# Performance work log

Hardware: AMD Instinct MI355X
Metric: run time of the kernel (lower is better)

The kernel has to match this reference:

```python
import jax, jax.numpy as jnp
import numpy as np

NEG_BIG = -9.0e15

def setup_inputs() -> dict:
    key = jax.random.key(0)
    k1, k2, k3, k4 = jax.random.split(key, 4)
    N, F_in, F_out = 2048, 512, 64
    x = jax.random.normal(k1, (N, F_in), dtype=jnp.float32)
    adj = jax.random.randint(k2, (N, N), 0, 2, dtype=jnp.int32)
    # xavier_uniform with gain=1.414
    def xavier(k, shape, gain=1.414):
        fan_in, fan_out = shape[0], shape[1]
        bound = gain * np.sqrt(6.0 / (fan_in + fan_out))
        return jax.random.uniform(k, shape, jnp.float32, -bound, bound)
    W = xavier(k3, (F_in, F_out))
    a = xavier(k4, (F_out, 1))
    return {"x": x, "adj": adj, "W": W, "a": a}

def reference(x, adj, W, a):
    h = x @ W                                  # [N, F_out]
    # pairwise |h_i - h_j| projected by a: e[i,j] = relu(sum_f |h_i,f - h_j,f| * a_f)
    diff = jnp.abs(h[:, None, :] - h[None, :, :])   # [N, N, F_out]
    e = jax.nn.relu(jnp.einsum('ijf,fo->ij', diff, a))  # [N, N]
    scores = jnp.where(adj > 0, e, NEG_BIG)
    attention = jax.nn.softmax(scores, axis=1)
    out = attention @ h                        # [N, F_out]
    return jax.nn.relu(out)                    # concat=True path
```

## Files before the change

### kernel.cpp

```cpp
#include <hip/hip_runtime.h>

#define Nn 2048
#define FIN 512
#define FO 64
#define SHIFT 20.0f
#define NSEG 4
#define SEGJ (Nn / NSEG)
#define CH 64
#define LST 66
#define PSTRIDE 68

__global__ __launch_bounds__(256) void gat_xw(const float* __restrict__ x,
                                              const float* __restrict__ W,
                                              float* __restrict__ h) {
    __shared__ float part[2][2][FO];
    const int wave = threadIdx.x >> 6;
    const int lane = threadIdx.x & 63;
    const int rs = wave >> 1;
    const int kh = wave & 1;
    int row = blockIdx.x * 2 + rs;
    row = __builtin_amdgcn_readfirstlane(row);
    const float* xr = x + (size_t)row * FIN + kh * (FIN / 2);
    const float* Wp = W + (size_t)kh * (FIN / 2) * FO;
    float acc = 0.f;
#pragma unroll 2
    for (int k = 0; k < FIN / 2; k += 8) {
        float4 xa = *(const float4*)(xr + k);
        float4 xb = *(const float4*)(xr + k + 4);
        acc = fmaf(xa.x, Wp[(k + 0) * FO + lane], acc);
        acc = fmaf(xa.y, Wp[(k + 1) * FO + lane], acc);
        acc = fmaf(xa.z, Wp[(k + 2) * FO + lane], acc);
        acc = fmaf(xa.w, Wp[(k + 3) * FO + lane], acc);
        acc = fmaf(xb.x, Wp[(k + 4) * FO + lane], acc);
        acc = fmaf(xb.y, Wp[(k + 5) * FO + lane], acc);
        acc = fmaf(xb.z, Wp[(k + 6) * FO + lane], acc);
        acc = fmaf(xb.w, Wp[(k + 7) * FO + lane], acc);
    }
    part[rs][kh][lane] = acc;
    __syncthreads();
    if (threadIdx.x < 128) {
        const int r2 = threadIdx.x >> 6;
        const int l2 = threadIdx.x & 63;
        h[((size_t)blockIdx.x * 2 + r2) * FO + l2] = part[r2][0][l2] + part[r2][1][l2];
    }
}

__global__ __launch_bounds__(256) void gat_attn(const float* __restrict__ h,
                                                const int* __restrict__ adj,
                                                const float* __restrict__ a,
                                                float* __restrict__ pws) {
    __shared__ float hj[CH * LST];
    __shared__ float hia[4 * FO * 2];
    const int tid = threadIdx.x;
    const int wave = tid >> 6;
    const int lane = tid & 63;
    const int seg = blockIdx.x & (NSEG - 1);
    const int row = (blockIdx.x >> 2) * 4 + wave;

    hia[wave * (FO * 2) + lane * 2]     = h[(size_t)row * FO + lane];
    hia[wave * (FO * 2) + lane * 2 + 1] = a[lane];

    float l = 0.f;
    float2 op2[32];
#pragma unroll
    for (int q = 0; q < 32; q++) op2[q] = make_float2(0.f, 0.f);

    const int* adjrow = adj + (size_t)row * Nn + seg * SEGJ;
    const float* hseg = h + (size_t)seg * SEGJ * FO;

    for (int j0 = 0; j0 < SEGJ; j0 += CH) {
        __syncthreads();
#pragma unroll
        for (int u = 0; u < 4; u++) {
            const int g4 = u * 256 + tid;
            const float4 v = *(const float4*)(hseg + (size_t)j0 * FO + (size_t)g4 * 4);
            float* dst = &hj[(g4 >> 4) * LST + (g4 & 15) * 4];
            ((float2*)dst)[0] = make_float2(v.x, v.y);
            *(float2*)(dst + 2) = make_float2(v.z, v.w);
        }
        __syncthreads();

        const int av = adjrow[j0 + lane];

        float2 hjv[32];
#pragma unroll
        for (int q = 0; q < 32; q++)
            hjv[q] = *(const float2*)&hj[lane * LST + q * 2];

        float e = 0.f;
#pragma unroll
        for (int q = 0; q < 32; q++) {
            const float4 c = *(const float4*)&hia[wave * (FO * 2) + q * 4];
            e = fmaf(fabsf(hjv[q].x - c.x), c.y, e);
            e = fmaf(fabsf(hjv[q].y - c.z), c.w, e);
        }

        const float pe = __expf(fmaxf(e, 0.f) - SHIFT);
        const float p = (av > 0) ? pe : 0.f;
        l += p;

#pragma unroll
        for (int q = 0; q < 32; q++) {
            op2[q].x = fmaf(p, hjv[q].x, op2[q].x);
            op2[q].y = fmaf(p, hjv[q].y, op2[q].y);
        }
    }

#pragma unroll
    for (int s = 32; s >= 1; s >>= 1) l += __shfl_xor(l, s, 64);
#pragma unroll
    for (int q = 0; q < 32; q++) {
        op2[q].x += __shfl_xor(op2[q].x, 16, 64);
        op2[q].x += __shfl_xor(op2[q].x, 32, 64);
        op2[q].y += __shfl_xor(op2[q].y, 16, 64);
        op2[q].y += __shfl_xor(op2[q].y, 32, 64);
    }
    __syncthreads();
    float* red = &hj[wave * (16 * 65)];
    if (lane < 16) {
#pragma unroll
        for (int q = 0; q < 32; q++) {
            red[lane * 65 + 2 * q]     = op2[q].x;
            red[lane * 65 + 2 * q + 1] = op2[q].y;
        }
    }
    float tot = 0.f;
#pragma unroll
    for (int g = 0; g < 16; g++)
        tot += red[g * 65 + lane];
    float* prow = pws + ((size_t)seg * Nn + row) * PSTRIDE;
    prow[lane] = tot;
    if (lane == 0) prow[FO] = l;
}

__global__ __launch_bounds__(256) void gat_merge(const float* __restrict__ pws,
                                                 float* __restrict__ out) {
    const int t = blockIdx.x * 256 + threadIdx.x;
    const int row = t >> 6;
    const int f = t & 63;
    float o = 0.f, l = 0.f;
#pragma unroll
    for (int s = 0; s < NSEG; s++) {
        const float* pr = pws + ((size_t)s * Nn + row) * PSTRIDE;
        o += pr[f];
        l += pr[FO];
    }
    out[t] = fmaxf(o / l, 0.f);
}

extern "C" void kernel_launch(void* const* d_in, const int* in_sizes, int n_in,
                              void* d_out, int out_size, void* d_ws, size_t ws_size,
                              hipStream_t stream) {
    const float* x   = (const float*)d_in[0];
    const int*   adj = (const int*)d_in[1];
    const float* W   = (const float*)d_in[2];
    const float* a   = (const float*)d_in[3];
    float* out = (float*)d_out;
    float* h   = (float*)d_ws;
    float* pws = (float*)d_ws + (size_t)Nn * FO;

    gat_xw<<<dim3(1024), dim3(256), 0, stream>>>(x, W, h);
    gat_attn<<<dim3(512 * NSEG), dim3(256), 0, stream>>>(h, adj, a, pws);
    gat_merge<<<dim3(512), dim3(256), 0, stream>>>(pws, out);
}
```

Baseline: 143.1 us.

## Register-tile attention as 64x128 i-j blocks with atomic accumulation

Replaces the one-row-per-wave attention kernel with a 2D tiled kernel. Each block owns 64 query rows and a 128-column key range, each thread computes a 4x4 patch of scores, and the probabilities are staged transposed in shared memory for a 4x4 register-tiled P·H product. This raises reuse of the h_i and h_j values loaded from shared memory, where the old code re-read every h_j once per row. Partial sums from the 16 column tiles go into global buffers through atomicAdd, after a new zeroing kernel clears them. The cost is an extra launch, atomic contention, float-order nondeterminism, and fewer blocks (512), which may leave the machine underfilled.

```diff
diff --git a/kernel.cpp b/kernel.cpp
--- a/kernel.cpp
+++ b/kernel.cpp
@@ -4,11 +4,14 @@
 #define FIN 512
 #define FO 64
 #define SHIFT 20.0f
-#define NSEG 4
-#define SEGJ (Nn / NSEG)
-#define CH 64
-#define LST 66
-#define PSTRIDE 68
+#define NJT 16
+#define JR (Nn / NJT)
+#define LS 66
+#define PTS 68
+
+__global__ __launch_bounds__(256) void gat_zero(float* __restrict__ z) {
+    z[blockIdx.x * 256 + threadIdx.x] = 0.f;
+}
 
 __global__ __launch_bounds__(256) void gat_xw(const float* __restrict__ x,
                                               const float* __restrict__ W,
@@ -45,107 +48,153 @@
     }
 }
 
-__global__ __launch_bounds__(256) void gat_attn(const float* __restrict__ h,
-                                                const int* __restrict__ adj,
-                                                const float* __restrict__ a,
-                                                float* __restrict__ pws) {
-    __shared__ float hj[CH * LST];
-    __shared__ float hia[4 * FO * 2];
+__global__ __launch_bounds__(256) void gat_attn3(const float* __restrict__ h,
+                                                 const int* __restrict__ adj,
+                                                 const float* __restrict__ a,
+                                                 float* __restrict__ osum,
+                                                 float* __restrict__ lsum) {
+    __shared__ float hi_s[64 * LS];
+    __shared__ float hj_s[64 * LS];
+    __shared__ float pT_s[64 * PTS];
+    __shared__ float a_s[FO];
+
     const int tid = threadIdx.x;
-    const int wave = tid >> 6;
+    const int w = tid >> 6;
     const int lane = tid & 63;
-    const int seg = blockIdx.x & (NSEG - 1);
-    const int row = (blockIdx.x >> 2) * 4 + wave;
-
-    hia[wave * (FO * 2) + lane * 2]     = h[(size_t)row * FO + lane];
-    hia[wave * (FO * 2) + lane * 2 + 1] = a[lane];
-
-    float l = 0.f;
-    float2 op2[32];
-#pragma unroll
-    for (int q = 0; q < 32; q++) op2[q] = make_float2(0.f, 0.f);
-
-    const int* adjrow = adj + (size_t)row * Nn + seg * SEGJ;
-    const float* hseg = h + (size_t)seg * SEGJ * FO;
-
-    for (int j0 = 0; j0 < SEGJ; j0 += CH) {
+    const int li = lane & 3;
+    const int lj = lane >> 2;
+    const int it = blockIdx.x >> 4;
+    const int jt = blockIdx.x & (NJT - 1);
+    const int ib = it * 64;
+    const int jb = jt * JR;
+    const int iw = w * 16;
+
+    for (int g4 = tid; g4 < 1024; g4 += 256) {
+        float4 v = *(const float4*)(h + (size_t)ib * FO + (size_t)g4 * 4);
+        float* d = &hi_s[(g4 >> 4) * LS + (g4 & 15) * 4];
+        *(float2*)d = make_float2(v.x, v.y);
+        *(float2*)(d + 2) = make_float2(v.z, v.w);
+    }
+    if (tid < FO) a_s[tid] = a[tid];
+
+    float pv[4][4];
+    float ls[4];
+#pragma unroll
+    for (int u = 0; u < 4; u++) {
+        ls[u] = 0.f;
+#pragma unroll
+        for (int v2 = 0; v2 < 4; v2++) pv[u][v2] = 0.f;
+    }
+
+    for (int jc = 0; jc < JR; jc += 64) {
         __syncthreads();
-#pragma unroll
-        for (int u = 0; u < 4; u++) {
-            const int g4 = u * 256 + tid;
-            const float4 v = *(const float4*)(hseg + (size_t)j0 * FO + (size_t)g4 * 4);
-            float* dst = &hj[(g4 >> 4) * LST + (g4 & 15) * 4];
-            ((float2*)dst)[0] = make_float2(v.x, v.y);
-            *(float2*)(dst + 2) = make_float2(v.z, v.w);
+        const float* hsrc = h + (size_t)(jb + jc) * FO;
+        for (int g4 = tid; g4 < 1024; g4 += 256) {
+            float4 v = *(const float4*)(hsrc + (size_t)g4 * 4);
+            float* d = &hj_s[(g4 >> 4) * LS + (g4 & 15) * 4];
+            *(float2*)d = make_float2(v.x, v.y);
+            *(float2*)(d + 2) = make_float2(v.z, v.w);
         }
         __syncthreads();
 
-        const int av = adjrow[j0 + lane];
-
-        float2 hjv[32];
-#pragma unroll
-        for (int q = 0; q < 32; q++)
-            hjv[q] = *(const float2*)&hj[lane * LST + q * 2];
-
-        float e = 0.f;
-#pragma unroll
-        for (int q = 0; q < 32; q++) {
-            const float4 c = *(const float4*)&hia[wave * (FO * 2) + q * 4];
-            e = fmaf(fabsf(hjv[q].x - c.x), c.y, e);
-            e = fmaf(fabsf(hjv[q].y - c.z), c.w, e);
-        }
-
-        const float pe = __expf(fmaxf(e, 0.f) - SHIFT);
-        const float p = (av > 0) ? pe : 0.f;
-        l += p;
-
-#pragma unroll
-        for (int q = 0; q < 32; q++) {
-            op2[q].x = fmaf(p, hjv[q].x, op2[q].x);
-            op2[q].y = fmaf(p, hjv[q].y, op2[q].y);
-        }
-    }
-
-#pragma unroll
-    for (int s = 32; s >= 1; s >>= 1) l += __shfl_xor(l, s, 64);
-#pragma unroll
-    for (int q = 0; q < 32; q++) {
-        op2[q].x += __shfl_xor(op2[q].x, 16, 64);
-        op2[q].x += __shfl_xor(op2[q].x, 32, 64);
-        op2[q].y += __shfl_xor(op2[q].y, 16, 64);
-        op2[q].y += __shfl_xor(op2[q].y, 32, 64);
-    }
-    __syncthreads();
-    float* red = &hj[wave * (16 * 65)];
-    if (lane < 16) {
-#pragma unroll
-        for (int q = 0; q < 32; q++) {
-            red[lane * 65 + 2 * q]     = op2[q].x;
-            red[lane * 65 + 2 * q + 1] = op2[q].y;
-        }
-    }
-    float tot = 0.f;
-#pragma unroll
-    for (int g = 0; g < 16; g++)
-        tot += red[g * 65 + lane];
-    float* prow = pws + ((size_t)seg * Nn + row) * PSTRIDE;
-    prow[lane] = tot;
-    if (lane == 0) prow[FO] = l;
-}
-
-__global__ __launch_bounds__(256) void gat_merge(const float* __restrict__ pws,
-                                                 float* __restrict__ out) {
+        int4 am[4];
+#pragma unroll
+        for (int di = 0; di < 4; di++)
+            am[di] = *(const int4*)(adj + (size_t)(ib + iw + 4 * li + di) * Nn + (jb + jc + 4 * lj));
+
+        float e[4][4];
+#pragma unroll
+        for (int di = 0; di < 4; di++)
+#pragma unroll
+            for (int dj = 0; dj < 4; dj++) e[di][dj] = 0.f;
+
+#pragma unroll 4
+        for (int f = 0; f < FO; f += 2) {
+            const float2 av = *(const float2*)&a_s[f];
+            float2 hi[4], hj[4];
+#pragma unroll
+            for (int d = 0; d < 4; d++) {
+                hi[d] = *(const float2*)&hi_s[(iw + 4 * li + d) * LS + f];
+                hj[d] = *(const float2*)&hj_s[(4 * lj + d) * LS + f];
+            }
+#pragma unroll
+            for (int di = 0; di < 4; di++)
+#pragma unroll
+                for (int dj = 0; dj < 4; dj++) {
+                    e[di][dj] = fmaf(fabsf(hi[di].x - hj[dj].x), av.x, e[di][dj]);
+                    e[di][dj] = fmaf(fabsf(hi[di].y - hj[dj].y), av.y, e[di][dj]);
+                }
+        }
+
+#pragma unroll
+        for (int di = 0; di < 4; di++) {
+            const int* ap = (const int*)&am[di];
+#pragma unroll
+            for (int dj = 0; dj < 4; dj++) {
+                const float p = (ap[dj] > 0) ? __expf(fmaxf(e[di][dj], 0.f) - SHIFT) : 0.f;
+                e[di][dj] = p;
+                ls[di] += p;
+            }
+        }
+
+#pragma unroll
+        for (int dj = 0; dj < 4; dj++) {
+            *(float4*)&pT_s[(4 * lj + dj) * PTS + iw + 4 * li] =
+                make_float4(e[0][dj], e[1][dj], e[2][dj], e[3][dj]);
+        }
+        __syncthreads();
+
+#pragma unroll 4
+        for (int j = 0; j < 64; j++) {
+            const float4 pj = *(const float4*)&pT_s[j * PTS + iw + 4 * li];
+            const float2 h0 = *(const float2*)&hj_s[j * LS + 4 * lj];
+            const float2 h1 = *(const float2*)&hj_s[j * LS + 4 * lj + 2];
+            pv[0][0] = fmaf(pj.x, h0.x, pv[0][0]);
+            pv[0][1] = fmaf(pj.x, h0.y, pv[0][1]);
+            pv[0][2] = fmaf(pj.x, h1.x, pv[0][2]);
+            pv[0][3] = fmaf(pj.x, h1.y, pv[0][3]);
+            pv[1][0] = fmaf(pj.y, h0.x, pv[1][0]);
+            pv[1][1] = fmaf(pj.y, h0.y, pv[1][1]);
+            pv[1][2] = fmaf(pj.y, h1.x, pv[1][2]);
+            pv[1][3] = fmaf(pj.y, h1.y, pv[1][3]);
+            pv[2][0] = fmaf(pj.z, h0.x, pv[2][0]);
+            pv[2][1] = fmaf(pj.z, h0.y, pv[2][1]);
+            pv[2][2] = fmaf(pj.z, h1.x, pv[2][2]);
+            pv[2][3] = fmaf(pj.z, h1.y, pv[2][3]);
+            pv[3][0] = fmaf(pj.w, h0.x, pv[3][0]);
+            pv[3][1] = fmaf(pj.w, h0.y, pv[3][1]);
+            pv[3][2] = fmaf(pj.w, h1.x, pv[3][2]);
+            pv[3][3] = fmaf(pj.w, h1.y, pv[3][3]);
+        }
+    }
+
+#pragma unroll
+    for (int di = 0; di < 4; di++) {
+        float v = ls[di];
+        v += __shfl_xor(v, 4, 64);
+        v += __shfl_xor(v, 8, 64);
+        v += __shfl_xor(v, 16, 64);
+        v += __shfl_xor(v, 32, 64);
+        ls[di] = v;
+    }
+    if (lj == 0) {
+#pragma unroll
+        for (int di = 0; di < 4; di++)
+            atomicAdd(&lsum[ib + iw + 4 * li + di], ls[di]);
+    }
+#pragma unroll
+    for (int di = 0; di < 4; di++) {
+#pragma unroll
+        for (int v2 = 0; v2 < 4; v2++)
+            atomicAdd(&osum[(size_t)(ib + iw + 4 * li + di) * FO + 4 * lj + v2], pv[di][v2]);
+    }
+}
+
+__global__ __launch_bounds__(256) void gat_fin(const float* __restrict__ osum,
+                                               const float* __restrict__ lsum,
+                                               float* __restrict__ out) {
     const int t = blockIdx.x * 256 + threadIdx.x;
-    const int row = t >> 6;
-    const int f = t & 63;
-    float o = 0.f, l = 0.f;
-#pragma unroll
-    for (int s = 0; s < NSEG; s++) {
-        const float* pr = pws + ((size_t)s * Nn + row) * PSTRIDE;
-        o += pr[f];
-        l += pr[FO];
-    }
-    out[t] = fmaxf(o / l, 0.f);
+    out[t] = fmaxf(osum[t] / lsum[t >> 6], 0.f);
 }
 
 extern "C" void kernel_launch(void* const* d_in, const int* in_sizes, int n_in,
@@ -156,10 +205,13 @@
     const float* W   = (const float*)d_in[2];
     const float* a   = (const float*)d_in[3];
     float* out = (float*)d_out;
-    float* h   = (float*)d_ws;
-    float* pws = (float*)d_ws + (size_t)Nn * FO;
-
+
+    float* h    = (float*)d_ws;
+    float* osum = h + (size_t)Nn * FO;
+    float* lsum = osum + (size_t)Nn * FO;
+
+    gat_zero<<<dim3(520), dim3(256), 0, stream>>>(osum);
     gat_xw<<<dim3(1024), dim3(256), 0, stream>>>(x, W, h);
-    gat_attn<<<dim3(512 * NSEG), dim3(256), 0, stream>>>(h, adj, a, pws);
-    gat_merge<<<dim3(512), dim3(256), 0, stream>>>(pws, out);
-}
+    gat_attn3<<<dim3(32 * NJT), dim3(256), 0, stream>>>(h, adj, a, osum, lsum);
+    gat_fin<<<dim3(512), dim3(256), 0, stream>>>(osum, lsum, out);
+}
```

Result: faster. 136.2 us (-4.8%).

## Tile attention over i×j blocks and compute P·H with split-bf16 MFMA

Applied to the files above, without the earlier changes.

Rewrites the attention kernel so each block handles a 16-row by 1024-column tile. Each thread computes scores for 8 rows by 2 columns, so every h_j loaded from swizzled LDS is reused across rows. The P·H product runs on bf16 MFMA using a hi/lo split (three MFMAs) to approximate fp32 accuracy. A new transpose kernel precomputes H^T in hi/lo bf16, and the merge now combines two column halves instead of four. The grid drops to 256 blocks, which risks underfilling the GPU, and h_i is read from global memory inside the inner loop.

```diff
diff --git a/kernel.cpp b/kernel.cpp
--- a/kernel.cpp
+++ b/kernel.cpp
@@ -4,11 +4,18 @@
 #define FIN 512
 #define FO 64
 #define SHIFT 20.0f
-#define NSEG 4
-#define SEGJ (Nn / NSEG)
-#define CH 64
-#define LST 66
-#define PSTRIDE 68
+#define NJT 2
+#define JSEG 1024
+#define CHK 256
+
+typedef __attribute__((ext_vector_type(8))) short bf16x8;
+typedef __attribute__((ext_vector_type(4))) float f32x4;
+
+__device__ __forceinline__ unsigned rne_bf16(float x) {
+    unsigned u = __float_as_uint(x);
+    return (u + 0x7FFFu + ((u >> 16) & 1u)) >> 16;
+}
+__device__ __forceinline__ float bf16_f32(unsigned s) { return __uint_as_float(s << 16); }
 
 __global__ __launch_bounds__(256) void gat_xw(const float* __restrict__ x,
                                               const float* __restrict__ W,
@@ -45,106 +52,145 @@
     }
 }
 
-__global__ __launch_bounds__(256) void gat_attn(const float* __restrict__ h,
-                                                const int* __restrict__ adj,
-                                                const float* __restrict__ a,
-                                                float* __restrict__ pws) {
-    __shared__ float hj[CH * LST];
-    __shared__ float hia[4 * FO * 2];
+__global__ __launch_bounds__(256) void gat_tr(const float* __restrict__ h,
+                                              unsigned short* __restrict__ hbT_hi,
+                                              unsigned short* __restrict__ hbT_lo) {
+    __shared__ float t_s[64 * 68];
     const int tid = threadIdx.x;
-    const int wave = tid >> 6;
+    const int j0 = blockIdx.x * 64;
+    for (int g4 = tid; g4 < 1024; g4 += 256) {
+        float4 v = *(const float4*)(h + (size_t)j0 * FO + (size_t)g4 * 4);
+        *(float4*)&t_s[(g4 >> 4) * 68 + (g4 & 15) * 4] = v;
+    }
+    __syncthreads();
+    const int f = tid >> 2, q = tid & 3;
+    unsigned* dh = (unsigned*)&hbT_hi[(size_t)f * Nn + j0 + q * 16];
+    unsigned* dl = (unsigned*)&hbT_lo[(size_t)f * Nn + j0 + q * 16];
+#pragma unroll
+    for (int u = 0; u < 8; u++) {
+        float x0 = t_s[(q * 16 + 2 * u) * 68 + f];
+        float x1 = t_s[(q * 16 + 2 * u + 1) * 68 + f];
+        unsigned h0 = rne_bf16(x0), h1 = rne_bf16(x1);
+        dh[u] = h0 | (h1 << 16);
+        float r0 = x0 - bf16_f32(h0), r1 = x1 - bf16_f32(h1);
+        dl[u] = rne_bf16(r0) | (rne_bf16(r1) << 16);
+    }
+}
+
+__global__ __launch_bounds__(256) void gat_attn7(const float* __restrict__ h,
+                                                 const int* __restrict__ adj,
+                                                 const float* __restrict__ a,
+                                                 const unsigned short* __restrict__ hbT_hi,
+                                                 const unsigned short* __restrict__ hbT_lo,
+                                                 float* __restrict__ opart,
+                                                 float* __restrict__ lpart) {
+    __shared__ float hj_s[CHK * 64];
+    __shared__ unsigned short Ph_s[16 * 264];
+    __shared__ unsigned short Pl_s[16 * 264];
+
+    const int tid = threadIdx.x;
+    const int it = blockIdx.x >> 1;
+    const int jt = blockIdx.x & 1;
+    const int ib = it * 16;
+    const int jb = jt * JSEG;
+    const int ig = __builtin_amdgcn_readfirstlane(tid >> 7);
+    const int jg = tid & 127;
     const int lane = tid & 63;
-    const int seg = blockIdx.x & (NSEG - 1);
-    const int row = (blockIdx.x >> 2) * 4 + wave;
-
-    hia[wave * (FO * 2) + lane * 2]     = h[(size_t)row * FO + lane];
-    hia[wave * (FO * 2) + lane * 2 + 1] = a[lane];
-
-    float l = 0.f;
-    float2 op2[32];
-#pragma unroll
-    for (int q = 0; q < 32; q++) op2[q] = make_float2(0.f, 0.f);
-
-    const int* adjrow = adj + (size_t)row * Nn + seg * SEGJ;
-    const float* hseg = h + (size_t)seg * SEGJ * FO;
-
-    for (int j0 = 0; j0 < SEGJ; j0 += CH) {
+    const int w = tid >> 6;
+    const int m = lane & 15;
+    const int g = lane >> 4;
+
+    float ls[8] = {0.f, 0.f, 0.f, 0.f, 0.f, 0.f, 0.f, 0.f};
+    f32x4 acc = {0.f, 0.f, 0.f, 0.f};
+
+    for (int jc = 0; jc < JSEG; jc += CHK) {
         __syncthreads();
-#pragma unroll
-        for (int u = 0; u < 4; u++) {
-            const int g4 = u * 256 + tid;
-            const float4 v = *(const float4*)(hseg + (size_t)j0 * FO + (size_t)g4 * 4);
-            float* dst = &hj[(g4 >> 4) * LST + (g4 & 15) * 4];
-            ((float2*)dst)[0] = make_float2(v.x, v.y);
-            *(float2*)(dst + 2) = make_float2(v.z, v.w);
+        const float* hsrc = h + (size_t)(jb + jc) * FO;
+        for (int g4 = tid; g4 < 4096; g4 += 256) {
+            const int j = g4 >> 4, c = g4 & 15;
+            *(float4*)&hj_s[j * 64 + ((c ^ (j & 7)) << 2)] =
+                *(const float4*)(hsrc + (size_t)g4 * 4);
         }
         __syncthreads();
 
-        const int av = adjrow[j0 + lane];
-
-        float2 hjv[32];
-#pragma unroll
-        for (int q = 0; q < 32; q++)
-            hjv[q] = *(const float2*)&hj[lane * LST + q * 2];
-
-        float e = 0.f;
-#pragma unroll
-        for (int q = 0; q < 32; q++) {
-            const float4 c = *(const float4*)&hia[wave * (FO * 2) + q * 4];
-            e = fmaf(fabsf(hjv[q].x - c.x), c.y, e);
-            e = fmaf(fabsf(hjv[q].y - c.z), c.w, e);
-        }
-
-        const float pe = __expf(fmaxf(e, 0.f) - SHIFT);
-        const float p = (av > 0) ? pe : 0.f;
-        l += p;
-
-#pragma unroll
-        for (int q = 0; q < 32; q++) {
-            op2[q].x = fmaf(p, hjv[q].x, op2[q].x);
-            op2[q].y = fmaf(p, hjv[q].y, op2[q].y);
-        }
-    }
-
-#pragma unroll
-    for (int s = 32; s >= 1; s >>= 1) l += __shfl_xor(l, s, 64);
-#pragma unroll
-    for (int q = 0; q < 32; q++) {
-        op2[q].x += __shfl_xor(op2[q].x, 16, 64);
-        op2[q].x += __shfl_xor(op2[q].x, 32, 64);
-        op2[q].y += __shfl_xor(op2[q].y, 16, 64);
-        op2[q].y += __shfl_xor(op2[q].y, 32, 64);
-    }
-    __syncthreads();
-    float* red = &hj[wave * (16 * 65)];
-    if (lane < 16) {
-#pragma unroll
-        for (int q = 0; q < 32; q++) {
-            red[lane * 65 + 2 * q]     = op2[q].x;
-            red[lane * 65 + 2 * q + 1] = op2[q].y;
-        }
-    }
-    float tot = 0.f;
-#pragma unroll
-    for (int g = 0; g < 16; g++)
-        tot += red[g * 65 + lane];
-    float* prow = pws + ((size_t)seg * Nn + row) * PSTRIDE;
-    prow[lane] = tot;
-    if (lane == 0) prow[FO] = l;
-}
-
-__global__ __launch_bounds__(256) void gat_merge(const float* __restrict__ pws,
+        const int j0 = jg * 2, j1 = j0 + 1;
+        int2 am[8];
+        const int* adjp = adj + (size_t)(ib + ig * 8) * Nn + (jb + jc + j0);
+#pragma unroll
+        for (int ii = 0; ii < 8; ii++) am[ii] = *(const int2*)(adjp + (size_t)ii * Nn);
+
+        float e[8][2];
+#pragma unroll
+        for (int ii = 0; ii < 8; ii++) e[ii][0] = e[ii][1] = 0.f;
+
+#pragma unroll 2
+        for (int fq = 0; fq < 16; fq++) {
+            const int f = fq * 4;
+            const float4 av = *(const float4*)(a + f);
+            const float4 hj0 = *(const float4*)&hj_s[j0 * 64 + ((fq ^ (j0 & 7)) << 2)];
+            const float4 hj1 = *(const float4*)&hj_s[j1 * 64 + ((fq ^ (j1 & 7)) << 2)];
+#pragma unroll
+            for (int ii = 0; ii < 8; ii++) {
+                const float4 hi = *(const float4*)(h + (size_t)(ib + ig * 8 + ii) * FO + f);
+                e[ii][0] = fmaf(fabsf(hi.x - hj0.x), av.x, e[ii][0]);
+                e[ii][0] = fmaf(fabsf(hi.y - hj0.y), av.y, e[ii][0]);
+                e[ii][0] = fmaf(fabsf(hi.z - hj0.z), av.z, e[ii][0]);
+                e[ii][0] = fmaf(fabsf(hi.w - hj0.w), av.w, e[ii][0]);
+                e[ii][1] = fmaf(fabsf(hi.x - hj1.x), av.x, e[ii][1]);
+                e[ii][1] = fmaf(fabsf(hi.y - hj1.y), av.y, e[ii][1]);
+                e[ii][1] = fmaf(fabsf(hi.z - hj1.z), av.z, e[ii][1]);
+                e[ii][1] = fmaf(fabsf(hi.w - hj1.w), av.w, e[ii][1]);
+            }
+        }
+
+#pragma unroll
+        for (int ii = 0; ii < 8; ii++) {
+            const float p0 = (am[ii].x > 0) ? __expf(fmaxf(e[ii][0], 0.f) - SHIFT) : 0.f;
+            const float p1 = (am[ii].y > 0) ? __expf(fmaxf(e[ii][1], 0.f) - SHIFT) : 0.f;
+            ls[ii] += p0 + p1;
+            const unsigned h0 = rne_bf16(p0), h1 = rne_bf16(p1);
+            const float r0 = p0 - bf16_f32(h0), r1 = p1 - bf16_f32(h1);
+            ((unsigned*)Ph_s)[(ig * 8 + ii) * 132 + jg] = h0 | (h1 << 16);
+            ((unsigned*)Pl_s)[(ig * 8 + ii) * 132 + jg] =
+                rne_bf16(r0) | (rne_bf16(r1) << 16);
+        }
+        __syncthreads();
+
+        const size_t bbase = (size_t)(w * 16 + m) * Nn + (jb + jc);
+#pragma unroll
+        for (int ks = 0; ks < 8; ks++) {
+            const bf16x8 af = *(const bf16x8*)&Ph_s[m * 264 + ks * 32 + g * 8];
+            const bf16x8 al = *(const bf16x8*)&Pl_s[m * 264 + ks * 32 + g * 8];
+            const bf16x8 bh = *(const bf16x8*)&hbT_hi[bbase + ks * 32 + g * 8];
+            const bf16x8 bl = *(const bf16x8*)&hbT_lo[bbase + ks * 32 + g * 8];
+            acc = __builtin_amdgcn_mfma_f32_16x16x32_bf16(af, bh, acc, 0, 0, 0);
+            acc = __builtin_amdgcn_mfma_f32_16x16x32_bf16(af, bl, acc, 0, 0, 0);
+            acc = __builtin_amdgcn_mfma_f32_16x16x32_bf16(al, bh, acc, 0, 0, 0);
+        }
+    }
+
+    __syncthreads();
+    float* red = hj_s;
+#pragma unroll
+    for (int ii = 0; ii < 8; ii++) red[(ig * 8 + ii) * 132 + jg] = ls[ii];
+    __syncthreads();
+    if (tid < 16) {
+        float l = 0.f;
+        for (int c2 = 0; c2 < 128; c2++) l += red[tid * 132 + c2];
+        lpart[(size_t)jt * Nn + ib + tid] = l;
+    }
+#pragma unroll
+    for (int r = 0; r < 4; r++)
+        opart[((size_t)jt * Nn + ib + g * 4 + r) * FO + w * 16 + m] = acc[r];
+}
+
+__global__ __launch_bounds__(256) void gat_merge(const float* __restrict__ opart,
+                                                 const float* __restrict__ lpart,
                                                  float* __restrict__ out) {
     const int t = blockIdx.x * 256 + threadIdx.x;
-    const int row = t >> 6;
-    const int f = t & 63;
-    float o = 0.f, l = 0.f;
-#pragma unroll
-    for (int s = 0; s < NSEG; s++) {
-        const float* pr = pws + ((size_t)s * Nn + row) * PSTRIDE;
-        o += pr[f];
-        l += pr[FO];
-    }
+    const int i = t >> 6;
+    const float o = opart[t] + opart[(size_t)Nn * FO + t];
+    const float l = lpart[i] + lpart[Nn + i];
     out[t] = fmaxf(o / l, 0.f);
 }
 
@@ -156,10 +202,15 @@
     const float* W   = (const float*)d_in[2];
     const float* a   = (const float*)d_in[3];
     float* out = (float*)d_out;
-    float* h   = (float*)d_ws;
-    float* pws = (float*)d_ws + (size_t)Nn * FO;
+
+    float* h     = (float*)d_ws;
+    float* opart = h + (size_t)Nn * FO;
+    float* lpart = opart + (size_t)NJT * Nn * FO;
+    unsigned short* hbT_hi = (unsigned short*)(lpart + (size_t)NJT * Nn);
+    unsigned short* hbT_lo = hbT_hi + (size_t)FO * Nn;
 
     gat_xw<<<dim3(1024), dim3(256), 0, stream>>>(x, W, h);
-    gat_attn<<<dim3(512 * NSEG), dim3(256), 0, stream>>>(h, adj, a, pws);
-    gat_merge<<<dim3(512), dim3(256), 0, stream>>>(pws, out);
-}
+    gat_tr<<<dim3(32), dim3(256), 0, stream>>>(h, hbT_hi, hbT_lo);
+    gat_attn7<<<dim3(256), dim3(256), 0, stream>>>(h, adj, a, hbT_hi, hbT_lo, opart, lpart);
+    gat_merge<<<dim3(512), dim3(256), 0, stream>>>(opart, lpart, out);
+}
```

Measured after the change: 140.3 us. Within noise of the previous version (-1.9%).
